# Optimization experiments

Hardware: AMD Instinct MI355X
Metric: run time of the kernel (lower is better)

Reference implementation:

```python
import jax, jax.numpy as jnp
import numpy as np

B, S, D = 4, 4096, 1024  # S = maxlength * 2, D = hidden_dim * 2 (bi-rnn)
MAXLENGTH = 2048
NEG_BIG = -2.0 ** 31


def setup_inputs() -> dict:
    key = jax.random.key(0)
    k1, k2, k3, k4, k5 = jax.random.split(key, 5)
    inputs = jax.random.normal(k1, (B, S, D), dtype=jnp.float32)
    length = jax.random.randint(k2, (B,), 1, MAXLENGTH + 1, dtype=jnp.int32)
    # torch code requires max(length)*2 == maxlength*2 for expand() to work
    length = length.at[0].set(MAXLENGTH)
    scale = 1.0 / np.sqrt(D)
    Wq = jax.random.normal(k3, (D, D), dtype=jnp.float32) * scale
    Wk = jax.random.normal(k4, (D, D), dtype=jnp.float32) * scale
    Wv = jax.random.normal(k5, (D, D), dtype=jnp.float32) * scale
    return {"inputs": inputs, "length": length, "Wq": Wq, "Wk": Wk,
            "Wv": Wv, "maxlength": MAXLENGTH}


def reference(inputs, length, Wq, Wk, Wv, maxlength):
    # nn.Linear (bias=False): y = x @ W.T
    Q = inputs @ Wq.T                      # [B, S, D]
    K = inputs @ Wk.T                      # [B, S, D]
    V = inputs @ Wv.T                      # [B, S, D]
    max_len = maxlength * 2
    sent_len = length.astype(jnp.float32) * 2.0      # [B]
    # key-padding mask, broadcast over query dim: [B, 1, max_len]
    mask = (jnp.arange(max_len, dtype=jnp.float32)[None, :] < sent_len[:, None])[:, None, :]
    alpha = jnp.einsum('bqd,bkd->bqk', Q, K)         # [B, S, S] (no 1/sqrt(d) scaling, as in source)
    alpha = jnp.where(mask, alpha, NEG_BIG)
    alpha = jax.nn.softmax(alpha, axis=2)
    out = jnp.einsum('bqk,bkd->bqd', alpha, V)       # [B, S, D]
    return out
```

## Files before the change

kernel.cpp:

```cpp
#include <hip/hip_runtime.h>


typedef __attribute__((ext_vector_type(4))) float floatx4;
typedef __attribute__((ext_vector_type(4))) int intx4;
typedef __attribute__((ext_vector_type(8))) short shortx8;
typedef unsigned short ushort_t;

__device__ __forceinline__ ushort_t f2bf(float f) {
  union { float f; unsigned u; } x; x.f = f;
  unsigned r = x.u + 0x7fffu + ((x.u >> 16) & 1u);
  return (ushort_t)(r >> 16);
}
__device__ __forceinline__ float bf2f(ushort_t h) {
  union { unsigned u; float f; } x; x.u = ((unsigned)h) << 16; return x.f;
}
__device__ __forceinline__ void quant8(float v, char& qh, char& ql) {
  float vs = v * 16.0f;
  float h = rintf(vs);
  h = fminf(fmaxf(h, -127.f), 127.f);
  float l = rintf((vs - h) * 256.0f);
  l = fminf(fmaxf(l, -127.f), 127.f);
  qh = (char)(int)h; ql = (char)(int)l;
}
__device__ __forceinline__ void quant8w(float v, char& qh, char& ql) {
  float vs = v * 512.0f;
  float h = rintf(vs);
  h = fminf(fmaxf(h, -127.f), 127.f);
  float l = rintf((vs - h) * 256.0f);
  l = fminf(fmaxf(l, -127.f), 127.f);
  qh = (char)(int)h; ql = (char)(int)l;
}

__device__ __forceinline__ void gload_lds16(const void* g, void* l) {
  __builtin_amdgcn_global_load_lds(
      (__attribute__((address_space(1))) void*)(uintptr_t)g,
      (__attribute__((address_space(3))) void*)(unsigned)(uintptr_t)l,
      16, 0, 0);
}

template<int N> __device__ __forceinline__ void wait_vm() {
  static_assert(N == 0 || N == 4 || N == 6 || N == 8 || N == 12, "bad vmcnt");
  if constexpr (N == 0)       asm volatile("s_waitcnt vmcnt(0)" ::: "memory");
  else if constexpr (N == 4)  asm volatile("s_waitcnt vmcnt(4)" ::: "memory");
  else if constexpr (N == 6)  asm volatile("s_waitcnt vmcnt(6)" ::: "memory");
  else if constexpr (N == 8)  asm volatile("s_waitcnt vmcnt(8)" ::: "memory");
  else if constexpr (N == 12) asm volatile("s_waitcnt vmcnt(12)" ::: "memory");
}
template<int NL> __device__ __forceinline__ void wait_chunk(int rem) {
  if (rem >= 2)      wait_vm<2 * NL>();
  else if (rem == 1) wait_vm<NL>();
  else               wait_vm<0>();
}
__device__ __forceinline__ void barrier_fenced() {
  asm volatile("" ::: "memory");
  __builtin_amdgcn_s_barrier();
  asm volatile("" ::: "memory");
}

template<int TM, int TN, int OMODE, int LMODE>
__global__ __launch_bounds__(256)
void gemm_bt(const ushort_t* __restrict__ A0g, const ushort_t* __restrict__ B0g,
             void* __restrict__ C0v, int K, int lda, int ldc, long bstride,
             const int* __restrict__ lenp, int b0)
{
  constexpr int BM = TM * 32, BN = TN * 32;
  constexpr int LA = TM / 2, LB = TN / 2;
  constexpr int NL = LA + LB;
  constexpr int BUFA = BM * 32, BUFB = BN * 32;
  __shared__ ushort_t As[3][BM][32];
  __shared__ ushort_t Bs[3][BN][32];

  const int tid = threadIdx.x;
  const long row0 = (long)blockIdx.x * BM;
  const long col0 = (long)blockIdx.y * BN;

  int kend = K;
  if constexpr (LMODE == 2) {
    const int sent = lenp[b0] * 2;
    kend = (sent + 127) & ~127;
  } else if constexpr (LMODE == 3) {
    const int sent = lenp[row0 >> 12] * 2;
    if ((int)(row0 & 4095) >= ((sent + 127) & ~127)) return;
  }

  const int sr = tid >> 2, scol = (tid & 3) * 8;
  const ushort_t* pA = A0g + (row0 + sr) * (long)lda + scol;
  const ushort_t* pB = B0g + (col0 + sr) * (long)K + scol;
  ushort_t* lA = &As[0][sr][scol];
  ushort_t* lB = &Bs[0][sr][scol];
  const long jA = 64 * (long)lda, jB = 64 * (long)K;

  const int wid = tid >> 6, lane = tid & 63;
  const int wm = (wid >> 1) * (BM / 2), wn = (wid & 1) * (BN / 2);
  const int lr = lane & 15, lq = lane >> 4;

  floatx4 acc[TM][TN] = {};

  auto stage = [&](int buf, int k0) {
#pragma unroll
    for (int j = 0; j < LA; ++j)
      gload_lds16(pA + k0 + j * jA, lA + buf * BUFA + j * 2048);
#pragma unroll
    for (int j = 0; j < LB; ++j)
      gload_lds16(pB + k0 + j * jB, lB + buf * BUFB + j * 2048);
  };

  const int nk = kend >> 5;
  stage(0, 0);
  stage(1, 32);
  int cur = 0, nx2 = 2;
  for (int t = 0; t < nk; ++t) {
    if (t + 2 < nk) stage(nx2, (t + 2) << 5);
    wait_chunk<NL>(nk - 1 - t);
    barrier_fenced();

    const ushort_t* Ab = &As[cur][0][0];
    const ushort_t* Bb = &Bs[cur][0][0];
    shortx8 af[TM], bf[TN];
#pragma unroll
    for (int tt = 0; tt < TM; ++tt)
      af[tt] = *(const shortx8*)&Ab[(wm + tt * 16 + lr) * 32 + lq * 8];
#pragma unroll
    for (int tt = 0; tt < TN; ++tt)
      bf[tt] = *(const shortx8*)&Bb[(wn + tt * 16 + lr) * 32 + lq * 8];
#pragma unroll
    for (int mt = 0; mt < TM; ++mt)
#pragma unroll
      for (int nt = 0; nt < TN; ++nt)
        acc[mt][nt] = __builtin_amdgcn_mfma_f32_16x16x32_bf16(af[mt], bf[nt], acc[mt][nt], 0, 0, 0);

    barrier_fenced();
    cur = (cur == 2) ? 0 : cur + 1;
    nx2 = (nx2 == 2) ? 0 : nx2 + 1;
  }

#pragma unroll
  for (int mt = 0; mt < TM; ++mt) {
#pragma unroll
    for (int nt = 0; nt < TN; ++nt) {
      long col = col0 + wn + nt * 16 + lr;
      if constexpr (OMODE == 2) {
        long row = row0 + wm + mt * 16 + lq * 4;
        long bb = row >> 12, s = row & 4095;
        ushort4 pk;
        pk.x = f2bf(acc[mt][nt][0]); pk.y = f2bf(acc[mt][nt][1]);
        pk.z = f2bf(acc[mt][nt][2]); pk.w = f2bf(acc[mt][nt][3]);
        *(ushort4*)&((ushort_t*)C0v)[bb * bstride + col * ldc + s] = pk;
      } else {
#pragma unroll
        for (int r = 0; r < 4; ++r) {
          long row = row0 + wm + mt * 16 + lq * 4 + r;
          ((float*)C0v)[row * ldc + col] = acc[mt][nt][r];
        }
      }
    }
  }
}

template<int LMODE>
__global__ __launch_bounds__(256)
void proj_i8(const char* __restrict__ Ah, const char* __restrict__ Al,
             const char* __restrict__ Bh, const char* __restrict__ Bl,
             char* __restrict__ Ch, char* __restrict__ Cl,
             const int* __restrict__ lenp)
{
  __shared__ char As[3][2][128][64];
  __shared__ char Bs[3][2][64][64];
  const int tid = threadIdx.x;
  const long row0 = (long)blockIdx.x * 128;
  const long col0 = (long)blockIdx.y * 64;
  if constexpr (LMODE == 3) {
    const int sent = lenp[row0 >> 12] * 2;
    if ((int)(row0 & 4095) >= ((sent + 127) & ~127)) return;
  }

  const int sr = tid >> 2, sc16 = (tid & 3) * 16;
  const char* pA0 = Ah + (row0 + sr) * 1024 + sc16;
  const char* pA1 = Al + (row0 + sr) * 1024 + sc16;
  const char* pB0 = Bh + (col0 + sr) * 1024 + sc16;
  const char* pB1 = Bl + (col0 + sr) * 1024 + sc16;
  char* lA0 = &As[0][0][sr][sc16];
  char* lA1 = &As[0][1][sr][sc16];
  char* lB0 = &Bs[0][0][sr][sc16];
  char* lB1 = &Bs[0][1][sr][sc16];

  const int wid = tid >> 6, lane = tid & 63;
  const int wm = (wid >> 1) * 64, wn = (wid & 1) * 32;
  const int lr = lane & 15, lq = lane >> 4;

  intx4 acc1[4][2] = {};
  intx4 acc2[4][2] = {};
  intx4 acc3[4][2] = {};

  auto stage = [&](int buf, int k0) {
#pragma unroll
    for (int j = 0; j < 2; ++j) {
      gload_lds16(pA0 + k0 + j * 65536, lA0 + buf * 16384 + j * 4096);
      gload_lds16(pA1 + k0 + j * 65536, lA1 + buf * 16384 + j * 4096);
    }
    gload_lds16(pB0 + k0, lB0 + buf * 8192);
    gload_lds16(pB1 + k0, lB1 + buf * 8192);
  };

  stage(0, 0);
  stage(1, 64);
  int cur = 0, nx2 = 2;
  for (int t = 0; t < 16; ++t) {
    if (t + 2 < 16) stage(nx2, (t + 2) << 6);
    wait_chunk<6>(15 - t);
    barrier_fenced();

    const char* Ab = &As[cur][0][0][0];
    const char* Bb = &Bs[cur][0][0][0];
    intx4 ah[4], al[4], bh[2], bl[2];
#pragma unroll
    for (int tt = 0; tt < 4; ++tt) {
      ah[tt] = *(const intx4*)&Ab[(wm + tt * 16 + lr) * 64 + lq * 16];
      al[tt] = *(const intx4*)&Ab[8192 + (wm + tt * 16 + lr) * 64 + lq * 16];
    }
#pragma unroll
    for (int tt = 0; tt < 2; ++tt) {
      bh[tt] = *(const intx4*)&Bb[(wn + tt * 16 + lr) * 64 + lq * 16];
      bl[tt] = *(const intx4*)&Bb[4096 + (wn + tt * 16 + lr) * 64 + lq * 16];
    }
#pragma unroll
    for (int mt = 0; mt < 4; ++mt)
#pragma unroll
      for (int nt = 0; nt < 2; ++nt) {
        acc1[mt][nt] = __builtin_amdgcn_mfma_i32_16x16x64_i8(ah[mt], bh[nt], acc1[mt][nt], 0, 0, 0);
        acc2[mt][nt] = __builtin_amdgcn_mfma_i32_16x16x64_i8(ah[mt], bl[nt], acc2[mt][nt], 0, 0, 0);
        acc2[mt][nt] = __builtin_amdgcn_mfma_i32_16x16x64_i8(al[mt], bh[nt], acc2[mt][nt], 0, 0, 0);
        acc3[mt][nt] = __builtin_amdgcn_mfma_i32_16x16x64_i8(al[mt], bl[nt], acc3[mt][nt], 0, 0, 0);
      }
    barrier_fenced();
    cur = (cur == 2) ? 0 : cur + 1;
    nx2 = (nx2 == 2) ? 0 : nx2 + 1;
  }

#pragma unroll
  for (int mt = 0; mt < 4; ++mt)
#pragma unroll
    for (int nt = 0; nt < 2; ++nt) {
      long col = col0 + wn + nt * 16 + lr;
#pragma unroll
      for (int r = 0; r < 4; ++r) {
        long row = row0 + wm + mt * 16 + lq * 4 + r;
        float v = ((float)acc1[mt][nt][r]
                   + (float)acc2[mt][nt][r] * (1.0f / 256.0f)
                   + (float)acc3[mt][nt][r] * (1.0f / 65536.0f)) * (1.0f / 8192.0f);
        char qh, ql;
        quant8(v, qh, ql);
        Ch[row * 1024 + col] = qh;
        Cl[row * 1024 + col] = ql;
      }
    }
}

__global__ __launch_bounds__(256)
void qk_i8(const char* __restrict__ Qh, const char* __restrict__ Ql,
           const char* __restrict__ Kh, const char* __restrict__ Kl,
           short* __restrict__ sc, const int* __restrict__ lenp, int b)
{
  __shared__ char As[3][2][128][64];
  __shared__ char Bs[3][2][64][64];
  const int tid = threadIdx.x;
  const long row0 = (long)blockIdx.x * 128;
  const long col0 = (long)blockIdx.y * 64;
  const int sent = lenp[b] * 2;
  if (col0 >= sent) return;

  const int sr = tid >> 2, sc16 = (tid & 3) * 16;
  const char* pA0 = Qh + (row0 + sr) * 1024 + sc16;
  const char* pA1 = Ql + (row0 + sr) * 1024 + sc16;
  const char* pB0 = Kh + (col0 + sr) * 1024 + sc16;
  const char* pB1 = Kl + (col0 + sr) * 1024 + sc16;
  char* lA0 = &As[0][0][sr][sc16];
  char* lA1 = &As[0][1][sr][sc16];
  char* lB0 = &Bs[0][0][sr][sc16];
  char* lB1 = &Bs[0][1][sr][sc16];

  const int wid = tid >> 6, lane = tid & 63;
  const int wm = (wid >> 1) * 64, wn = (wid & 1) * 32;
  const int lr = lane & 15, lq = lane >> 4;

  intx4 acc1[4][2] = {};
  intx4 acc2[4][2] = {};

  auto stage = [&](int buf, int k0) {
#pragma unroll
    for (int j = 0; j < 2; ++j) {
      gload_lds16(pA0 + k0 + j * 65536, lA0 + buf * 16384 + j * 4096);
      gload_lds16(pA1 + k0 + j * 65536, lA1 + buf * 16384 + j * 4096);
    }
    gload_lds16(pB0 + k0, lB0 + buf * 8192);
    gload_lds16(pB1 + k0, lB1 + buf * 8192);
  };

  stage(0, 0);
  stage(1, 64);
  int cur = 0, nx2 = 2;
  for (int t = 0; t < 16; ++t) {
    if (t + 2 < 16) stage(nx2, (t + 2) << 6);
    wait_chunk<6>(15 - t);
    barrier_fenced();

    const char* Ab = &As[cur][0][0][0];
    const char* Bb = &Bs[cur][0][0][0];
    intx4 ah[4], al[4], bh[2], bl[2];
#pragma unroll
    for (int tt = 0; tt < 4; ++tt) {
      ah[tt] = *(const intx4*)&Ab[(wm + tt * 16 + lr) * 64 + lq * 16];
      al[tt] = *(const intx4*)&Ab[8192 + (wm + tt * 16 + lr) * 64 + lq * 16];
    }
#pragma unroll
    for (int tt = 0; tt < 2; ++tt) {
      bh[tt] = *(const intx4*)&Bb[(wn + tt * 16 + lr) * 64 + lq * 16];
      bl[tt] = *(const intx4*)&Bb[4096 + (wn + tt * 16 + lr) * 64 + lq * 16];
    }
#pragma unroll
    for (int mt = 0; mt < 4; ++mt)
#pragma unroll
      for (int nt = 0; nt < 2; ++nt) {
        acc1[mt][nt] = __builtin_amdgcn_mfma_i32_16x16x64_i8(ah[mt], bh[nt], acc1[mt][nt], 0, 0, 0);
        acc2[mt][nt] = __builtin_amdgcn_mfma_i32_16x16x64_i8(ah[mt], bl[nt], acc2[mt][nt], 0, 0, 0);
        acc2[mt][nt] = __builtin_amdgcn_mfma_i32_16x16x64_i8(al[mt], bh[nt], acc2[mt][nt], 0, 0, 0);
      }
    barrier_fenced();
    cur = (cur == 2) ? 0 : cur + 1;
    nx2 = (nx2 == 2) ? 0 : nx2 + 1;
  }

#pragma unroll
  for (int mt = 0; mt < 4; ++mt)
#pragma unroll
    for (int nt = 0; nt < 2; ++nt) {
      long col = col0 + wn + nt * 16 + lr;
#pragma unroll
      for (int r = 0; r < 4; ++r) {
        long row = row0 + wm + mt * 16 + lq * 4 + r;
        float v = (float)acc1[mt][nt][r] * 0.125f
                + (float)acc2[mt][nt][r] * (1.0f / 2048.0f);
        v = fminf(fmaxf(v, -32000.0f), 32000.0f);
        sc[row * 4096 + col] = (short)(int)rintf(v);
      }
    }
}

__global__ __launch_bounds__(256)
void cast_split(const float* __restrict__ in, ushort_t* __restrict__ hi,
                char* __restrict__ qh, char* __restrict__ ql, int n4) {
  int i = blockIdx.x * 256 + threadIdx.x;
  if (i < n4) {
    float4 v = ((const float4*)in)[i];
    ushort4 h;
    h.x = f2bf(v.x); h.y = f2bf(v.y); h.z = f2bf(v.z); h.w = f2bf(v.w);
    ((ushort4*)hi)[i] = h;
    char ax, bx, ay, by, az, bz, aw, bw;
    quant8(v.x, ax, bx); quant8(v.y, ay, by);
    quant8(v.z, az, bz); quant8(v.w, aw, bw);
    char4 a, b;
    a.x = ax; a.y = ay; a.z = az; a.w = aw;
    b.x = bx; b.y = by; b.z = bz; b.w = bw;
    ((char4*)qh)[i] = a;
    ((char4*)ql)[i] = b;
  }
}

__global__ __launch_bounds__(256)
void cast_wqk(const float* __restrict__ w0, const float* __restrict__ w1,
              char* __restrict__ h0, char* __restrict__ l0,
              char* __restrict__ h1, char* __restrict__ l1, int n4) {
  int i = blockIdx.x * 256 + threadIdx.x;
  if (i >= n4) return;
  const float* in = blockIdx.y ? w1 : w0;
  char* hp = blockIdx.y ? h1 : h0;
  char* lp = blockIdx.y ? l1 : l0;
  float4 v = ((const float4*)in)[i];
  char ax, bx, ay, by, az, bz, aw, bw;
  quant8w(v.x, ax, bx); quant8w(v.y, ay, by);
  quant8w(v.z, az, bz); quant8w(v.w, aw, bw);
  char4 a, b;
  a.x = ax; a.y = ay; a.z = az; a.w = aw;
  b.x = bx; b.y = by; b.z = bz; b.w = bw;
  ((char4*)hp)[i] = a;
  ((char4*)lp)[i] = b;
}

__global__ __launch_bounds__(256)
void cast_wv(const float* __restrict__ w, ushort_t* __restrict__ h, int n4) {
  int i = blockIdx.x * 256 + threadIdx.x;
  if (i >= n4) return;
  float4 v = ((const float4*)w)[i];
  ushort4 p;
  p.x = f2bf(v.x); p.y = f2bf(v.y); p.z = f2bf(v.z); p.w = f2bf(v.w);
  ((ushort4*)h)[i] = p;
}

__global__ __launch_bounds__(256)
void softmax_rows(short* __restrict__ scores, const int* __restrict__ length, int b0) {
  const long row = blockIdx.x;
  const int b = b0 + (int)(row >> 12);
  short* p = scores + row * 4096;
  const int sent = length[b] * 2;
  const int sentceil = (sent + 127) & ~127;
  const int tid = threadIdx.x;
  float vals[16];
  float mx = -3.4e38f;
  int nj = 0;
  for (int c = tid; c < sentceil; c += 256) {
    float v = (float)p[c] * (1.0f / 32.0f);
    v = (c < sent) ? v : -2147483648.0f;
    vals[nj++] = v;
    mx = fmaxf(mx, v);
  }
#pragma unroll
  for (int off = 32; off > 0; off >>= 1) mx = fmaxf(mx, __shfl_down(mx, off));
  __shared__ float red[8];
  if ((tid & 63) == 0) red[tid >> 6] = mx;
  __syncthreads();
  mx = fmaxf(fmaxf(red[0], red[1]), fmaxf(red[2], red[3]));
  float sum = 0.f;
  for (int j = 0; j < nj; ++j) { vals[j] = __expf(vals[j] - mx); sum += vals[j]; }
#pragma unroll
  for (int off = 32; off > 0; off >>= 1) sum += __shfl_down(sum, off);
  __syncthreads();
  if ((tid & 63) == 0) red[tid >> 6] = sum;
  __syncthreads();
  float inv = 1.0f / (red[0] + red[1] + red[2] + red[3]);
  ushort_t* pb = (ushort_t*)p;
  int j = 0;
  for (int c = tid; c < sentceil; c += 256) pb[c] = f2bf(vals[j++] * inv);
}

extern "C" void kernel_launch(void* const* d_in, const int* in_sizes, int n_in,
                              void* d_out, int out_size, void* d_ws, size_t ws_size,
                              hipStream_t stream) {
  const float* X   = (const float*)d_in[0];
  const int*   len = (const int*)d_in[1];
  const float* Wq  = (const float*)d_in[2];
  const float* Wk  = (const float*)d_in[3];
  const float* Wv  = (const float*)d_in[4];
  float* out = (float*)d_out;

  const int Bn = 4, S = 4096, D = 1024;
  const long MS = (long)Bn * S;

  char* w = (char*)d_ws;
  ushort_t* Xhi = (ushort_t*)w; w += MS * D * 2;
  char* Xh8 = w; w += MS * D;
  char* Xl8 = w; w += MS * D;
  char* Qh8 = w; w += MS * D;
  char* Ql8 = w; w += MS * D;
  char* Kh8 = w; w += MS * D;
  char* Kl8 = w; w += MS * D;
  ushort_t* Vt  = (ushort_t*)w; w += MS * D * 2;
  char* Wqh8 = w; w += (long)D * D;
  char* Wql8 = w; w += (long)D * D;
  char* Wkh8 = w; w += (long)D * D;
  char* Wkl8 = w; w += (long)D * D;
  ushort_t* Wvh = (ushort_t*)w; w += (long)D * D * 2;
  short* sc = (short*)d_ws;

  const int n4x = (int)(MS * D / 4);
  const int n4w = D * D / 4;
  cast_split<<<(n4x + 255) / 256, 256, 0, stream>>>(X, Xhi, Xh8, Xl8, n4x);
  cast_wqk<<<dim3((n4w + 255) / 256, 2), 256, 0, stream>>>(
      Wq, Wk, Wqh8, Wql8, Wkh8, Wkl8, n4w);
  cast_wv<<<(n4w + 255) / 256, 256, 0, stream>>>(Wv, Wvh, n4w);

  dim3 blk(256);
  proj_i8<0><<<dim3(MS / 128, D / 64), blk, 0, stream>>>(
      Xh8, Xl8, Wqh8, Wql8, Qh8, Ql8, len);
  proj_i8<3><<<dim3(MS / 128, D / 64), blk, 0, stream>>>(
      Xh8, Xl8, Wkh8, Wkl8, Kh8, Kl8, len);
  gemm_bt<4, 4, 2, 3><<<dim3(MS / 128, D / 128), blk, 0, stream>>>(
      Xhi, Wvh, Vt, D, D, S, (long)D * S, len, 0);

  for (int b = 0; b < Bn; ++b) {
    const long so = (long)b * S * D;
    qk_i8<<<dim3(S / 128, S / 64), blk, 0, stream>>>(
        Qh8 + so, Ql8 + so, Kh8 + so, Kl8 + so, sc, len, b);
    softmax_rows<<<S, 256, 0, stream>>>(sc, len, b);
    gemm_bt<4, 4, 0, 2><<<dim3(S / 128, D / 128), blk, 0, stream>>>(
        (const ushort_t*)sc, Vt + (long)b * D * S, out + so, S, S, D, 0, len, b);
  }
}
```

Measured before the change: 639.8 us.

## Merge Q/K int8 projections into one launch, double-buffer, narrower PV tiles

```diff
diff --git a/kernel.cpp b/kernel.cpp
--- a/kernel.cpp
+++ b/kernel.cpp
@@ -39,8 +39,10 @@
 }
 
 template<int N> __device__ __forceinline__ void wait_vm() {
-  static_assert(N == 0 || N == 4 || N == 6 || N == 8 || N == 12, "bad vmcnt");
+  static_assert(N == 0 || N == 3 || N == 4 || N == 6 || N == 8 || N == 12,
+                "bad vmcnt");
   if constexpr (N == 0)       asm volatile("s_waitcnt vmcnt(0)" ::: "memory");
+  else if constexpr (N == 3)  asm volatile("s_waitcnt vmcnt(3)" ::: "memory");
   else if constexpr (N == 4)  asm volatile("s_waitcnt vmcnt(4)" ::: "memory");
   else if constexpr (N == 6)  asm volatile("s_waitcnt vmcnt(6)" ::: "memory");
   else if constexpr (N == 8)  asm volatile("s_waitcnt vmcnt(8)" ::: "memory");
@@ -157,19 +159,20 @@
   }
 }
 
-template<int LMODE>
 __global__ __launch_bounds__(256)
 void proj_i8(const char* __restrict__ Ah, const char* __restrict__ Al,
              const char* __restrict__ Bh, const char* __restrict__ Bl,
-             char* __restrict__ Ch, char* __restrict__ Cl,
+             char* __restrict__ CQh, char* __restrict__ CQl,
+             char* __restrict__ CKh, char* __restrict__ CKl,
              const int* __restrict__ lenp)
 {
-  __shared__ char As[3][2][128][64];
-  __shared__ char Bs[3][2][64][64];
+  __shared__ char As[2][2][128][64];
+  __shared__ char Bs[2][2][64][64];
   const int tid = threadIdx.x;
   const long row0 = (long)blockIdx.x * 128;
   const long col0 = (long)blockIdx.y * 64;
-  if constexpr (LMODE == 3) {
+  const bool isK = col0 >= 1024;
+  if (isK) {
     const int sent = lenp[row0 >> 12] * 2;
     if ((int)(row0 & 4095) >= ((sent + 127) & ~127)) return;
   }
@@ -203,11 +206,10 @@
   };
 
   stage(0, 0);
-  stage(1, 64);
-  int cur = 0, nx2 = 2;
   for (int t = 0; t < 16; ++t) {
-    if (t + 2 < 16) stage(nx2, (t + 2) << 6);
-    wait_chunk<6>(15 - t);
+    const int cur = t & 1;
+    if (t + 1 < 16) { stage(cur ^ 1, (t + 1) << 6); wait_vm<6>(); }
+    else           { wait_vm<0>(); }
     barrier_fenced();
 
     const char* Ab = &As[cur][0][0][0];
@@ -233,15 +235,16 @@
         acc3[mt][nt] = __builtin_amdgcn_mfma_i32_16x16x64_i8(al[mt], bl[nt], acc3[mt][nt], 0, 0, 0);
       }
     barrier_fenced();
-    cur = (cur == 2) ? 0 : cur + 1;
-    nx2 = (nx2 == 2) ? 0 : nx2 + 1;
-  }
-
+  }
+
+  char* __restrict__ Ch = isK ? CKh : CQh;
+  char* __restrict__ Cl = isK ? CKl : CQl;
+  const long cbase = col0 & 1023;
 #pragma unroll
   for (int mt = 0; mt < 4; ++mt)
 #pragma unroll
     for (int nt = 0; nt < 2; ++nt) {
-      long col = col0 + wn + nt * 16 + lr;
+      long col = cbase + wn + nt * 16 + lr;
 #pragma unroll
       for (int r = 0; r < 4; ++r) {
         long row = row0 + wm + mt * 16 + lq * 4 + r;
@@ -454,10 +457,8 @@
   char* Kh8 = w; w += MS * D;
   char* Kl8 = w; w += MS * D;
   ushort_t* Vt  = (ushort_t*)w; w += MS * D * 2;
-  char* Wqh8 = w; w += (long)D * D;
-  char* Wql8 = w; w += (long)D * D;
-  char* Wkh8 = w; w += (long)D * D;
-  char* Wkl8 = w; w += (long)D * D;
+  char* WH8 = w; w += (long)2 * D * D;
+  char* WL8 = w; w += (long)2 * D * D;
   ushort_t* Wvh = (ushort_t*)w; w += (long)D * D * 2;
   short* sc = (short*)d_ws;
 
@@ -465,14 +466,12 @@
   const int n4w = D * D / 4;
   cast_split<<<(n4x + 255) / 256, 256, 0, stream>>>(X, Xhi, Xh8, Xl8, n4x);
   cast_wqk<<<dim3((n4w + 255) / 256, 2), 256, 0, stream>>>(
-      Wq, Wk, Wqh8, Wql8, Wkh8, Wkl8, n4w);
+      Wq, Wk, WH8, WL8, WH8 + (long)D * D, WL8 + (long)D * D, n4w);
   cast_wv<<<(n4w + 255) / 256, 256, 0, stream>>>(Wv, Wvh, n4w);
 
   dim3 blk(256);
-  proj_i8<0><<<dim3(MS / 128, D / 64), blk, 0, stream>>>(
-      Xh8, Xl8, Wqh8, Wql8, Qh8, Ql8, len);
-  proj_i8<3><<<dim3(MS / 128, D / 64), blk, 0, stream>>>(
-      Xh8, Xl8, Wkh8, Wkl8, Kh8, Kl8, len);
+  proj_i8<<<dim3(MS / 128, 2 * D / 64), blk, 0, stream>>>(
+      Xh8, Xl8, WH8, WL8, Qh8, Ql8, Kh8, Kl8, len);
   gemm_bt<4, 4, 2, 3><<<dim3(MS / 128, D / 128), blk, 0, stream>>>(
       Xhi, Wvh, Vt, D, D, S, (long)D * S, len, 0);
 
@@ -481,7 +480,7 @@
     qk_i8<<<dim3(S / 128, S / 64), blk, 0, stream>>>(
         Qh8 + so, Ql8 + so, Kh8 + so, Kl8 + so, sc, len, b);
     softmax_rows<<<S, 256, 0, stream>>>(sc, len, b);
-    gemm_bt<4, 4, 0, 2><<<dim3(S / 128, D / 128), blk, 0, stream>>>(
+    gemm_bt<4, 2, 0, 2><<<dim3(S / 128, D / 64), blk, 0, stream>>>(
         (const ushort_t*)sc, Vt + (long)b * D * S, out + so, S, S, D, 0, len, b);
   }
 }
```

Result: no change. 629.0 us (-1.7%).
